# Kernel optimization log

Hardware: AMD Instinct MI355X
Metric: run time of the kernel (lower is better)

Reference implementation:

```python
import jax, jax.numpy as jnp
import numpy as np

SEMA_DIM = 1024
L1, L2, B = 256, 320, 64


def setup_inputs() -> dict:
    key = jax.random.key(0)
    k1, k2, kw1, kb1, kw2, kb2 = jax.random.split(key, 6)
    D = SEMA_DIM
    s = 1.0 / np.sqrt(D)
    return {
        "r1": jax.random.normal(k1, (L1, B, D), dtype=jnp.float32),
        "r2": jax.random.normal(k2, (L2, B, D), dtype=jnp.float32),
        "W1": jax.random.uniform(kw1, (D, D), jnp.float32, -s, s),
        "b1": jax.random.uniform(kb1, (D,), jnp.float32, -s, s),
        "W2": jax.random.uniform(kw2, (D, D), jnp.float32, -s, s),
        "b2": jax.random.uniform(kb2, (D,), jnp.float32, -s, s),
    }


def _mlp(x, W1, b1, W2, b2):
    # torch Linear: x @ W.T + b
    h = jax.nn.relu(x @ W1.T + b1)
    return h @ W2.T + b2


def reference(r1, r2, W1, b1, W2, b2):
    # (L, B, D) -> mlp -> (B, L, D)
    r1 = jnp.transpose(_mlp(r1, W1, b1, W2, b2), (1, 0, 2))  # [B, L1, D]
    r2 = jnp.transpose(_mlp(r2, W1, b1, W2, b2), (1, 0, 2))  # [B, L2, D]

    o = jnp.einsum("bid,bjd->bij", r1, r2)  # [B, L1, L2]
    o1 = jax.nn.softmax(o, axis=2)           # attend r1 -> r2
    o2 = jax.nn.softmax(o, axis=1)           # attend r2 -> r1

    r1_c = jnp.einsum("bij,bjd->bid", o1, r2)  # [B, L1, D]
    r2_c = jnp.einsum("bij,bid->bjd", o2, r1)  # [B, L2, D]

    r1_pool = jnp.concatenate([r1, r1_c], axis=-1).sum(axis=1) / r1.shape[1]  # [B, 2D]
    r2_pool = jnp.concatenate([r2, r2_c], axis=-1).sum(axis=1) / r2.shape[1]  # [B, 2D]
    return (r1_pool, r2_pool)
```

## Files before the change

kernel.cpp:

```cpp
#include <hip/hip_runtime.h>
#include <stdint.h>

#define L1C 256
#define L2C 320
#define BC  64
#define DC  1024

typedef __bf16 bf16_t;
typedef __bf16 bf16x8 __attribute__((ext_vector_type(8)));
typedef __bf16 bf16x4 __attribute__((ext_vector_type(4)));
typedef float  f32x4  __attribute__((ext_vector_type(4)));

__device__ __forceinline__ void gload16(const void* g, void* l) {
  __builtin_amdgcn_global_load_lds(
      (__attribute__((address_space(1))) void*)g,
      (__attribute__((address_space(3))) void*)l, 16, 0, 0);
}

__global__ __launch_bounds__(256)
void prep_kernel(const float* __restrict__ r1, const float* __restrict__ r2,
                 bf16_t* __restrict__ XB,
                 const float* __restrict__ W1, bf16_t* __restrict__ WB1,
                 const float* __restrict__ W2, bf16_t* __restrict__ WB2,
                 bf16_t* __restrict__ W2T,
                 const float* __restrict__ b2, float* __restrict__ w2b,
                 float* __restrict__ zb) {
  __shared__ float buf[32 * 33];
  const int b = (int)blockIdx.x;
  if (b < 9216) {
    const float* src;
    size_t soff;
    if (b < 4096) { src = r1; soff = (size_t)b * 1024; }
    else          { src = r2; soff = (size_t)(b - 4096) * 1024; }
    const size_t doff = (size_t)b * 1024;
#pragma unroll
    for (int k = 0; k < 4; ++k) {
      const int i = threadIdx.x + k * 256;
      float4 v = ((const float4*)src)[soff + i];
      bf16x4 o = { (__bf16)v.x, (__bf16)v.y, (__bf16)v.z, (__bf16)v.w };
      ((bf16x4*)XB)[doff + i] = o;
    }
  } else if (b < 9728) {
    const int bb = b - 9216;
    const float* src = (bb < 256) ? W1 : W2;
    bf16_t* dst = (bb < 256) ? WB1 : WB2;
    const size_t base = (size_t)(bb & 255) * 1024;
#pragma unroll
    for (int k = 0; k < 4; ++k) {
      const int i = threadIdx.x + k * 256;
      float4 v = ((const float4*)src)[base + i];
      bf16x4 o = { (__bf16)v.x, (__bf16)v.y, (__bf16)v.z, (__bf16)v.w };
      ((bf16x4*)dst)[base + i] = o;
    }
  } else if (b < 10752) {
    const int bb = b - 9728;
    float (*tile)[33] = (float(*)[33])buf;
    const int tx = threadIdx.x & 31, ty = threadIdx.x >> 5;
    const int x0 = (bb & 31) * 32, y0 = (bb >> 5) * 32;
#pragma unroll
    for (int k = 0; k < 32; k += 8)
      tile[ty + k][tx] = W2[(size_t)(y0 + ty + k) * 1024 + x0 + tx];
    __syncthreads();
#pragma unroll
    for (int k = 0; k < 32; k += 8)
      W2T[(size_t)(x0 + ty + k) * 1024 + y0 + tx] = (bf16_t)tile[tx][ty + k];
  } else if (b < 10816) {
    const int bb = b - 10752;
    float (*red)[17] = (float(*)[17])buf;
    const int dt = threadIdx.x & 15, kg = threadIdx.x >> 4;
    const int d = bb * 16 + dt;
    float s = 0.f;
    for (int k = kg * 64; k < kg * 64 + 64; ++k)
      s += W2[(size_t)k * 1024 + d] * b2[k];
    red[kg][dt] = s;
    __syncthreads();
    if (kg == 0) {
      float t = 0.f;
#pragma unroll
      for (int g = 0; g < 16; ++g) t += red[g][dt];
      w2b[d] = t;
    }
  } else {
#pragma unroll
    for (int k = 0; k < 4; ++k) zb[threadIdx.x + k * 256] = 0.f;
  }
}

__global__ __launch_bounds__(256, 3)
void gemm1_128(const bf16_t* __restrict__ A, const bf16_t* __restrict__ W,
               const float* __restrict__ bias, bf16_t* __restrict__ C) {
  const int wg = ((int)blockIdx.x & 7) * 288 + ((int)blockIdx.x >> 3);
  const int mt = wg >> 3, nt = wg & 7;

  __shared__ __align__(16) char lds[49152];

  const int t = threadIdx.x;
  const int lane = t & 63, w = t >> 6;
  const int sRow = t >> 2;
  const int sCol8 = (((t & 3) ^ ((t >> 3) & 3))) * 8;
  const int t16 = t * 16;

  const bf16_t* A0 = A + (size_t)(mt * 128 + sRow) * 1024 + sCol8;
  const bf16_t* A1 = A0 + (size_t)64 * 1024;
  const bf16_t* B0 = W + (size_t)(nt * 128 + sRow) * 1024 + sCol8;
  const bf16_t* B1 = B0 + (size_t)64 * 1024;

  const int wr = (w >> 1) * 64, wc = (w & 1) * 64;
  const int rsel = lane & 15, hi = lane >> 4;
  const int kchunk = (hi ^ ((rsel >> 1) & 3)) << 4;
  const int offA = ((wr + rsel) << 6) + kchunk;
  const int offB = 8192 + ((wc + rsel) << 6) + kchunk;

  f32x4 acc[4][4] = {};

#pragma unroll
  for (int p = 0; p < 2; ++p) {
    char* db = lds + p * 16384;
    gload16(A0 + p * 32, db + t16);
    gload16(A1 + p * 32, db + 4096 + t16);
    gload16(B0 + p * 32, db + 8192 + t16);
    gload16(B1 + p * 32, db + 12288 + t16);
  }
  asm volatile("s_waitcnt vmcnt(4)" ::: "memory");
  __builtin_amdgcn_s_barrier();
  __builtin_amdgcn_sched_barrier(0);

  int cur = 0;
#pragma unroll 1
  for (int tt = 0; tt < 32; ++tt) {
    const char* rb = lds + cur * 16384;
    int nx = cur + 2; if (nx >= 3) nx -= 3;
    char* sb = lds + nx * 16384;
    const int ks = (tt + 2) * 32;
    bf16x8 af[4], bfv[4];
#pragma unroll
    for (int m = 0; m < 4; ++m) af[m] = *(const bf16x8*)(rb + offA + m * 1024);
#pragma unroll
    for (int n = 0; n < 4; ++n) bfv[n] = *(const bf16x8*)(rb + offB + n * 1024);
    if (tt < 30) {
      gload16(A0 + ks, sb + t16);
      gload16(A1 + ks, sb + 4096 + t16);
      gload16(B0 + ks, sb + 8192 + t16);
      gload16(B1 + ks, sb + 12288 + t16);
    }
    __builtin_amdgcn_s_setprio(1);
#pragma unroll
    for (int m = 0; m < 4; ++m)
#pragma unroll
      for (int n = 0; n < 4; ++n)
        acc[m][n] = __builtin_amdgcn_mfma_f32_16x16x32_bf16(af[m], bfv[n], acc[m][n], 0, 0, 0);
    __builtin_amdgcn_s_setprio(0);
    if (tt < 30)       asm volatile("s_waitcnt vmcnt(4)" ::: "memory");
    else if (tt == 30) asm volatile("s_waitcnt vmcnt(0)" ::: "memory");
    __builtin_amdgcn_s_barrier();
    __builtin_amdgcn_sched_barrier(0);
    cur = (cur + 1 == 3) ? 0 : cur + 1;
  }

  const int row0 = mt * 128 + wr + hi * 4;
  const int col0 = nt * 128 + wc + rsel;
  float bv[4];
#pragma unroll
  for (int n = 0; n < 4; ++n) bv[n] = bias[col0 + n * 16];
#pragma unroll
  for (int m = 0; m < 4; ++m) {
#pragma unroll
    for (int q = 0; q < 4; ++q) {
      const size_t rr = (size_t)(row0 + m * 16 + q) * 1024;
#pragma unroll
      for (int n = 0; n < 4; ++n) {
        float v = fmaxf(acc[m][n][q] + bv[n], 0.f);
        C[rr + col0 + n * 16] = (bf16_t)v;
      }
    }
  }
}

__global__ __launch_bounds__(256)
void tg_kernel(const bf16_t* __restrict__ H, const float* __restrict__ w2b,
               float* __restrict__ tT1, float* __restrict__ tT2,
               const bf16_t* __restrict__ W2T, float* __restrict__ Gpart) {
  __shared__ __align__(16) bf16_t sA[128 * 32];
  __shared__ __align__(16) bf16_t sB[128 * 32];
  const int blk = (int)blockIdx.x;
  if (blk >= 256) {
    const int wv = threadIdx.x >> 6, lane = threadIdx.x & 63;
    const int r = (blk - 256) * 4 + wv;
    const bf16_t* hrow = H + (size_t)r * 1024;
    float s = 0.f;
#pragma unroll
    for (int h = 0; h < 2; ++h) {
      bf16x8 v = *(const bf16x8*)(hrow + h * 512 + lane * 8);
#pragma unroll
      for (int e = 0; e < 8; ++e) s += (float)v[e] * w2b[h * 512 + lane * 8 + e];
    }
#pragma unroll
    for (int off = 32; off; off >>= 1) s += __shfl_xor(s, off);
    if (lane == 0) {
      const int b = r & 63;
      if (r < 16384) tT1[b * L1C + (r >> 6)] = s;
      else           tT2[b * L2C + ((r - 16384) >> 6)] = s;
    }
    return;
  }
  const int slice = blk >> 6;
  const int tl = blk & 63;
  const int mt = tl >> 3, nt = tl & 7;
  const int koff = slice * 256;

  const int f = threadIdx.x;
  const int lane = f & 63, w = f >> 6;
  const int sRow = f >> 2, sCol8 = (f & 3) * 8;

  const bf16_t* Ab = W2T + (size_t)mt * 128 * 1024 + (size_t)sRow * 1024 + sCol8;
  const bf16_t* Bb = W2T + (size_t)nt * 128 * 1024 + (size_t)sRow * 1024 + sCol8;

  bf16_t* sAp = sA + sRow * 32 + sCol8;
  bf16_t* sBp = sB + sRow * 32 + sCol8;

  const int wr = (w >> 1) * 64, wc = (w & 1) * 64;
  const int rsel = lane & 15, koff2 = (lane >> 4) * 8;
  const bf16_t* rA = sA + (wr + rsel) * 32 + koff2;
  const bf16_t* rB = sB + (wc + rsel) * 32 + koff2;

  f32x4 acc[4][4] = {};
  for (int kt = koff; kt < koff + 256; kt += 32) {
    __syncthreads();
    gload16(Ab + kt,             sAp);
    gload16(Ab + kt + 64 * 1024, sAp + 64 * 32);
    gload16(Bb + kt,             sBp);
    gload16(Bb + kt + 64 * 1024, sBp + 64 * 32);
    asm volatile("s_waitcnt vmcnt(0)" ::: "memory");
    __syncthreads();
    bf16x8 af[4], bfv[4];
#pragma unroll
    for (int m = 0; m < 4; ++m) af[m] = *(const bf16x8*)(rA + m * 16 * 32);
#pragma unroll
    for (int n = 0; n < 4; ++n) bfv[n] = *(const bf16x8*)(rB + n * 16 * 32);
#pragma unroll
    for (int m = 0; m < 4; ++m)
#pragma unroll
      for (int n = 0; n < 4; ++n)
        acc[m][n] = __builtin_amdgcn_mfma_f32_16x16x32_bf16(af[m], bfv[n], acc[m][n], 0, 0, 0);
  }

  float* Pb = Gpart + (size_t)slice * 1048576;
  const int row0 = mt * 128 + wr + (lane >> 4) * 4;
  const int col0 = nt * 128 + wc + rsel;
#pragma unroll
  for (int n = 0; n < 4; ++n) {
    const int c = col0 + n * 16;
#pragma unroll
    for (int m = 0; m < 4; ++m) {
      const int r = row0 + m * 16;
#pragma unroll
      for (int q = 0; q < 4; ++q)
        Pb[(size_t)(r + q) * 1024 + c] = acc[m][n][q];
    }
  }
}

__global__ __launch_bounds__(256)
void g_reduce(const float* __restrict__ Gp, bf16_t* __restrict__ GB) {
  const int i4 = blockIdx.x * 256 + threadIdx.x;
  float4 a = ((const float4*)Gp)[i4];
  float4 b = ((const float4*)(Gp + 1048576))[i4];
  float4 c = ((const float4*)(Gp + 2097152))[i4];
  float4 d = ((const float4*)(Gp + 3145728))[i4];
  bf16x4 o = { (bf16_t)(a.x + b.x + c.x + d.x), (bf16_t)(a.y + b.y + c.y + d.y),
               (bf16_t)(a.z + b.z + c.z + d.z), (bf16_t)(a.w + b.w + c.w + d.w) };
  ((bf16x4*)GB)[i4] = o;
}

__global__ __launch_bounds__(512, 2)
void mlp_gemm8(const bf16_t* __restrict__ A, const bf16_t* __restrict__ W,
               const float* __restrict__ bias, bf16_t* __restrict__ C,
               int Mtiles, int relu) {
  const int nwg = Mtiles * 4;
  const int cpx = nwg >> 3;
  const int wg  = ((int)blockIdx.x & 7) * cpx + ((int)blockIdx.x >> 3);
  const int mt = wg >> 2, nt = wg & 3;

  __shared__ __align__(16) char lds[131072];

  const int t    = threadIdx.x;
  const int lane = t & 63, wid = t >> 6;
  const int wm = wid >> 2, wn = wid & 3;
  const int rsel = lane & 15, hi = lane >> 4;
  const int t16 = t * 16;

  const int P0 = t16, P1 = 8192 + t16;
  const int Lg0 = P0 ^ ((P0 >> 3) & 0x30);
  const int Lg1 = P1 ^ ((P1 >> 3) & 0x30);
  const int rS0 = Lg0 >> 6, cS0 = (Lg0 & 63) >> 1;
  const int rS1 = Lg1 >> 6, cS1 = (Lg1 & 63) >> 1;
  const bf16_t* pA0 = A + (size_t)(mt * 256 + rS0) * 1024 + cS0;
  const bf16_t* pA1 = A + (size_t)(mt * 256 + rS1) * 1024 + cS1;
  const bf16_t* pB0 = W + (size_t)(nt * 256 + rS0) * 1024 + cS0;
  const bf16_t* pB1 = W + (size_t)(nt * 256 + rS1) * 1024 + cS1;

  const int kchunk = (hi ^ ((rsel >> 1) & 3)) << 4;
  const int offA = ((wm * 128 + rsel) << 6) + kchunk;
  const int offB = 16384 + ((wn * 64 + rsel) << 6) + kchunk;

  f32x4 acc[8][4] = {};
  bf16x8 bfr[4];

#pragma unroll
  for (int p = 0; p < 3; ++p) {
    char* db = lds + p * 32768;
    gload16(pA0 + p * 32, db + t16);
    gload16(pA1 + p * 32, db + 8192 + t16);
    gload16(pB0 + p * 32, db + 16384 + t16);
    gload16(pB1 + p * 32, db + 24576 + t16);
  }
  asm volatile("s_waitcnt vmcnt(8)" ::: "memory");
  __builtin_amdgcn_s_barrier();
  __builtin_amdgcn_sched_barrier(0);

#pragma unroll 1
  for (int tt = 0; tt < 32; ++tt) {
    const char* rb = lds + (tt & 3) * 32768;
    char* sb = lds + ((tt + 3) & 3) * 32768;
    const int ks = (tt + 3) * 32;
    bf16x8 af[4];
#pragma unroll
    for (int m = 0; m < 4; ++m) af[m] = *(const bf16x8*)(rb + offA + m * 1024);
#pragma unroll
    for (int n = 0; n < 4; ++n) bfr[n] = *(const bf16x8*)(rb + offB + n * 1024);
    if (tt < 29) {
      gload16(pA0 + ks, sb + t16);
      gload16(pA1 + ks, sb + 8192 + t16);
    }
    __builtin_amdgcn_s_setprio(1);
#pragma unroll
    for (int m = 0; m < 4; ++m)
#pragma unroll
      for (int n = 0; n < 4; ++n)
        acc[m][n] = __builtin_amdgcn_mfma_f32_16x16x32_bf16(af[m], bfr[n], acc[m][n], 0, 0, 0);
    __builtin_amdgcn_s_setprio(0);
    __builtin_amdgcn_s_barrier();
    __builtin_amdgcn_sched_barrier(0);
#pragma unroll
    for (int m = 0; m < 4; ++m) af[m] = *(const bf16x8*)(rb + offA + (m + 4) * 1024);
    if (tt < 29) {
      gload16(pB0 + ks, sb + 16384 + t16);
      gload16(pB1 + ks, sb + 24576 + t16);
    }
    __builtin_amdgcn_s_setprio(1);
#pragma unroll
    for (int m = 0; m < 4; ++m)
#pragma unroll
      for (int n = 0; n < 4; ++n)
        acc[m + 4][n] = __builtin_amdgcn_mfma_f32_16x16x32_bf16(af[m], bfr[n], acc[m + 4][n], 0, 0, 0);
    __builtin_amdgcn_s_setprio(0);
    if (tt < 29)       asm volatile("s_waitcnt vmcnt(8)" ::: "memory");
    else if (tt == 29) asm volatile("s_waitcnt vmcnt(4)" ::: "memory");
    else if (tt == 30) asm volatile("s_waitcnt vmcnt(0)" ::: "memory");
    __builtin_amdgcn_s_barrier();
    __builtin_amdgcn_sched_barrier(0);
  }

  const int row0 = mt * 256 + wm * 128 + hi * 4;
  const int col0 = nt * 256 + wn * 64 + rsel;
  float bv[4];
#pragma unroll
  for (int n = 0; n < 4; ++n) bv[n] = bias[col0 + n * 16];
#pragma unroll
  for (int m = 0; m < 8; ++m) {
#pragma unroll
    for (int q = 0; q < 4; ++q) {
      const size_t rr = (size_t)(row0 + m * 16 + q) * 1024;
#pragma unroll
      for (int n = 0; n < 4; ++n) {
        float v = acc[m][n][q] + bv[n];
        if (relu) v = fmaxf(v, 0.f);
        C[rr + col0 + n * 16] = (bf16_t)v;
      }
    }
  }
}

__global__ __launch_bounds__(256)
void pool_gemmK(const bf16_t* __restrict__ A, const bf16_t* __restrict__ W,
                float* __restrict__ P) {
  const int slice = (int)blockIdx.x >> 4;
  const int tl = (int)blockIdx.x & 15;
  const int mt = tl >> 3, nt = tl & 7;
  const int koff = slice * 128;

  const int f = threadIdx.x;
  const int lane = f & 63, w = f >> 6;
  const int sRow = f >> 2, sCol8 = (f & 3) * 8;

  const bf16_t* Ab = A + (size_t)mt * 128 * 1024 + (size_t)sRow * 1024 + sCol8;
  const bf16_t* Bb = W + (size_t)nt * 128 * 1024 + (size_t)sRow * 1024 + sCol8;

  __shared__ __align__(16) bf16_t sA[128 * 32];
  __shared__ __align__(16) bf16_t sB[128 * 32];
  bf16_t* sAp = sA + sRow * 32 + sCol8;
  bf16_t* sBp = sB + sRow * 32 + sCol8;

  const int wr = (w >> 1) * 64, wc = (w & 1) * 64;
  const int rsel = lane & 15, koff2 = (lane >> 4) * 8;
  const bf16_t* rA = sA + (wr + rsel) * 32 + koff2;
  const bf16_t* rB = sB + (wc + rsel) * 32 + koff2;

  f32x4 acc[4][4] = {};
  for (int kt = koff; kt < koff + 128; kt += 32) {
    __syncthreads();
    gload16(Ab + kt,             sAp);
    gload16(Ab + kt + 64 * 1024, sAp + 64 * 32);
    gload16(Bb + kt,             sBp);
    gload16(Bb + kt + 64 * 1024, sBp + 64 * 32);
    asm volatile("s_waitcnt vmcnt(0)" ::: "memory");
    __syncthreads();
    bf16x8 af[4], bfv[4];
#pragma unroll
    for (int m = 0; m < 4; ++m) af[m] = *(const bf16x8*)(rA + m * 16 * 32);
#pragma unroll
    for (int n = 0; n < 4; ++n) bfv[n] = *(const bf16x8*)(rB + n * 16 * 32);
#pragma unroll
    for (int m = 0; m < 4; ++m)
#pragma unroll
      for (int n = 0; n < 4; ++n)
        acc[m][n] = __builtin_amdgcn_mfma_f32_16x16x32_bf16(af[m], bfv[n], acc[m][n], 0, 0, 0);
  }

  float* Pb = P + (size_t)slice * 262144;
  const int row0 = mt * 128 + wr + (lane >> 4) * 4;
  const int col0 = nt * 128 + wc + rsel;
#pragma unroll
  for (int n = 0; n < 4; ++n) {
    const int c = col0 + n * 16;
#pragma unroll
    for (int m = 0; m < 4; ++m) {
      const int r = row0 + m * 16;
#pragma unroll
      for (int q = 0; q < 4; ++q)
        Pb[(size_t)(r + q) * 1024 + c] = acc[m][n][q];
    }
  }
}

__global__ __launch_bounds__(256)
void pool_reduce(const float* __restrict__ Pp, const float* __restrict__ b2,
                 float* __restrict__ out) {
  const int idx = blockIdx.x * 256 + threadIdx.x;
  const int r = idx >> 10, c = idx & 1023;
  float s = b2[c];
#pragma unroll
  for (int sl = 0; sl < 8; ++sl) s += Pp[(size_t)sl * 262144 + idx];
  const int g = r >> 6, b = r & 63;
  out[(size_t)(g >> 1) * 131072 + (size_t)b * 2048 + (g & 1) * 1024 + c] = s;
}

__global__ __launch_bounds__(256)
void logits_gemm(const bf16_t* __restrict__ Y1, const bf16_t* __restrict__ Y2,
                 float* __restrict__ O) {
  const int wg = ((int)blockIdx.x & 7) * 48 + ((int)blockIdx.x >> 3);
  const int b = wg / 6, t6 = wg % 6;
  const int mt = t6 / 3, nt = t6 % 3;

  __shared__ __align__(16) char lds[65536];

  const int t = threadIdx.x;
  const int lane = t & 63, w = t >> 6;
  const int sRow = t >> 2;
  const int sCol8 = (((t & 3) ^ ((t >> 3) & 3))) * 8;
  const int t16 = t * 16;

  const int i0 = mt * 128 + sRow;
  const int i1 = i0 + 64;
  int j0 = nt * 128 + sRow;      if (j0 > L2C - 1) j0 = L2C - 1;
  int j1 = nt * 128 + sRow + 64; if (j1 > L2C - 1) j1 = L2C - 1;
  const bf16_t* A0 = Y1 + ((size_t)i0 * BC + b) * DC + sCol8;
  const bf16_t* A1 = Y1 + ((size_t)i1 * BC + b) * DC + sCol8;
  const bf16_t* B0 = Y2 + ((size_t)j0 * BC + b) * DC + sCol8;
  const bf16_t* B1 = Y2 + ((size_t)j1 * BC + b) * DC + sCol8;

  const int wr = (w >> 1) * 64, wc = (w & 1) * 64;
  const int rsel = lane & 15, hi = lane >> 4;
  const int kchunk = (hi ^ ((rsel >> 1) & 3)) << 4;
  const int offA = ((wr + rsel) << 6) + kchunk;
  const int offB = 8192 + ((wc + rsel) << 6) + kchunk;

  f32x4 acc[4][4] = {};

#pragma unroll
  for (int p = 0; p < 3; ++p) {
    char* db = lds + p * 16384;
    gload16(A0 + p * 32, db + t16);
    gload16(A1 + p * 32, db + 4096 + t16);
    gload16(B0 + p * 32, db + 8192 + t16);
    gload16(B1 + p * 32, db + 12288 + t16);
  }
  asm volatile("s_waitcnt vmcnt(8)" ::: "memory");
  __builtin_amdgcn_s_barrier();
  __builtin_amdgcn_sched_barrier(0);

#pragma unroll 1
  for (int tt = 0; tt < 32; ++tt) {
    const char* rb = lds + (tt & 3) * 16384;
    char* sb = lds + ((tt + 3) & 3) * 16384;
    const int ks = (tt + 3) * 32;
    bf16x8 af[4], bfv[4];
#pragma unroll
    for (int m = 0; m < 4; ++m) af[m] = *(const bf16x8*)(rb + offA + m * 1024);
#pragma unroll
    for (int n = 0; n < 4; ++n) bfv[n] = *(const bf16x8*)(rb + offB + n * 1024);
    if (tt < 29) {
      gload16(A0 + ks, sb + t16);
      gload16(A1 + ks, sb + 4096 + t16);
      gload16(B0 + ks, sb + 8192 + t16);
      gload16(B1 + ks, sb + 12288 + t16);
    }
    __builtin_amdgcn_s_setprio(1);
#pragma unroll
    for (int m = 0; m < 4; ++m)
#pragma unroll
      for (int n = 0; n < 4; ++n)
        acc[m][n] = __builtin_amdgcn_mfma_f32_16x16x32_bf16(af[m], bfv[n], acc[m][n], 0, 0, 0);
    __builtin_amdgcn_s_setprio(0);
    if (tt < 29)       asm volatile("s_waitcnt vmcnt(8)" ::: "memory");
    else if (tt == 29) asm volatile("s_waitcnt vmcnt(4)" ::: "memory");
    else if (tt == 30) asm volatile("s_waitcnt vmcnt(0)" ::: "memory");
    __builtin_amdgcn_s_barrier();
    __builtin_amdgcn_sched_barrier(0);
  }

  float* Ob = O + (size_t)b * L1C * L2C;
  const int row0 = mt * 128 + wr + hi * 4;
  const int col0 = nt * 128 + wc + rsel;
#pragma unroll
  for (int n = 0; n < 4; ++n) {
    const int c = col0 + n * 16;
    if (c < L2C) {
#pragma unroll
      for (int m = 0; m < 4; ++m) {
        const int r = row0 + m * 16;
#pragma unroll
        for (int q = 0; q < 4; ++q)
          Ob[(size_t)(r + q) * L2C + c] = acc[m][n][q];
      }
    }
  }
}

__global__ __launch_bounds__(256)
void row_stats(const float* __restrict__ O, const float* __restrict__ tT2,
               float* __restrict__ rowM, float* __restrict__ rowInv) {
  const int gw = blockIdx.x * 4 + (threadIdx.x >> 6);
  const int lane = threadIdx.x & 63;
  const int b = gw >> 8;
  const float* row = O + (size_t)gw * L2C;
  const float* t2 = tT2 + b * L2C;
  float v[5];
  float m = -1e30f;
#pragma unroll
  for (int t = 0; t < 5; ++t) { v[t] = row[t * 64 + lane] + t2[t * 64 + lane]; m = fmaxf(m, v[t]); }
#pragma unroll
  for (int off = 32; off; off >>= 1) m = fmaxf(m, __shfl_xor(m, off));
  float s = 0.f;
#pragma unroll
  for (int t = 0; t < 5; ++t) s += __expf(v[t] - m);
#pragma unroll
  for (int off = 32; off; off >>= 1) s += __shfl_xor(s, off);
  if (lane == 0) { rowM[gw] = m; rowInv[gw] = 1.f / s; }
}

__global__ __launch_bounds__(256)
void col_stats_c1(const float* __restrict__ O, const float* __restrict__ tT1,
                  const float* __restrict__ tT2,
                  const float* __restrict__ rowM, const float* __restrict__ rowInv,
                  float* __restrict__ colM, float* __restrict__ colInv,
                  float* __restrict__ c1) {
  const int b = blockIdx.x / 5, jb = blockIdx.x % 5;
  const int jl = threadIdx.x & 63, ig = threadIdx.x >> 6;
  const int j = jb * 64 + jl;
  const float* Ob = O + (size_t)b * L1C * L2C + j;
  const float* rM = rowM + b * L1C;
  const float* rI = rowInv + b * L1C;
  const float* t1 = tT1 + b * L1C;
  const float t2j = tT2[b * L2C + j];
  float m = -1e30f, s = 0.f, cp = 0.f;
  for (int i = ig; i < L1C; i += 4) {
    float ov = Ob[(size_t)i * L2C];
    float v = ov + t1[i];
    float mn = fmaxf(m, v);
    s = s * __expf(m - mn) + __expf(v - mn);
    m = mn;
    cp += __expf(ov + t2j - rM[i]) * rI[i];
  }
  __shared__ float sm[4][64], ss[4][64], sc[4][64];
  sm[ig][jl] = m; ss[ig][jl] = s; sc[ig][jl] = cp;
  __syncthreads();
  if (ig == 0) {
    for (int g = 1; g < 4; ++g) {
      float mg = sm[g][jl], sg = ss[g][jl];
      float mn = fmaxf(m, mg);
      s = s * __expf(m - mn) + sg * __expf(mg - mn);
      m = mn;
      cp += sc[g][jl];
    }
    colM[b * L2C + j] = m;
    colInv[b * L2C + j] = 1.f / s;
    c1[b * L2C + j] = cp;
  }
}

__global__ __launch_bounds__(256)
void c2_kernel(const float* __restrict__ O, const float* __restrict__ tT1,
               const float* __restrict__ colM, const float* __restrict__ colInv,
               float* __restrict__ c2) {
  const int gw = blockIdx.x * 4 + (threadIdx.x >> 6);
  const int lane = threadIdx.x & 63;
  const int b = gw >> 8;
  const float* row = O + (size_t)gw * L2C;
  const float* cM = colM + b * L2C;
  const float* cI = colInv + b * L2C;
  const float t1i = tT1[b * L1C + (gw & 255)];
  float s = 0.f;
#pragma unroll
  for (int t = 0; t < 5; ++t) {
    const int j = t * 64 + lane;
    s += __expf(row[j] + t1i - cM[j]) * cI[j];
  }
#pragma unroll
  for (int off = 32; off; off >>= 1) s += __shfl_xor(s, off);
  if (lane == 0) c2[gw] = s;
}

__global__ __launch_bounds__(256)
void u_kernel(const bf16_t* __restrict__ H, const float* __restrict__ c1,
              const float* __restrict__ c2, bf16_t* __restrict__ Ub) {
  const int b = blockIdx.x >> 2;
  const int d = (blockIdx.x & 3) * 256 + threadIdx.x;
  const bf16_t* H2 = H + (size_t)L1C * BC * DC;
  float s1 = 0.f, s1c = 0.f, s2 = 0.f, s2c = 0.f;
  const float* c2b = c2 + b * L1C;
  for (int i = 0; i < L1C; ++i) {
    float v = (float)H[((size_t)i * BC + b) * DC + d];
    s1 += v; s1c += c2b[i] * v;
  }
  const float* c1b = c1 + b * L2C;
  for (int j = 0; j < L2C; ++j) {
    float v = (float)H2[((size_t)j * BC + b) * DC + d];
    s2 += v; s2c += c1b[j] * v;
  }
  Ub[(size_t)(0 * 64 + b) * 1024 + d] = (bf16_t)(s1  * (1.f / L1C));
  Ub[(size_t)(1 * 64 + b) * 1024 + d] = (bf16_t)(s2c * (1.f / L1C));
  Ub[(size_t)(2 * 64 + b) * 1024 + d] = (bf16_t)(s2  * (1.f / L2C));
  Ub[(size_t)(3 * 64 + b) * 1024 + d] = (bf16_t)(s1c * (1.f / L2C));
}

extern "C" void kernel_launch(void* const* d_in, const int* in_sizes, int n_in,
                              void* d_out, int out_size, void* d_ws, size_t ws_size,
                              hipStream_t stream) {
  const float* r1 = (const float*)d_in[0];
  const float* r2 = (const float*)d_in[1];
  const float* W1 = (const float*)d_in[2];
  const float* b1 = (const float*)d_in[3];
  const float* W2 = (const float*)d_in[4];
  const float* b2 = (const float*)d_in[5];
  float* out = (float*)d_out;
  char* ws = (char*)d_ws;

  const size_t M1 = (size_t)L1C * BC;
  const size_t M2 = (size_t)L2C * BC;
  const size_t Mt = M1 + M2;

  size_t off = 0;
  bf16_t* XB  = (bf16_t*)(ws + off); off += Mt * DC * 2;
  bf16_t* HB  = (bf16_t*)(ws + off); off += Mt * DC * 2;
  bf16_t* WB1 = (bf16_t*)(ws + off); off += (size_t)DC * DC * 2;
  bf16_t* WB2 = (bf16_t*)(ws + off); off += (size_t)DC * DC * 2;
  bf16_t* W2T = (bf16_t*)(ws + off); off += (size_t)DC * DC * 2;
  bf16_t* GB  = (bf16_t*)(ws + off); off += (size_t)DC * DC * 2;
  float* w2b   = (float*)(ws + off); off += 4096;
  float* zb    = (float*)(ws + off); off += 4096;
  float* tT1   = (float*)(ws + off); off += BC * L1C * 4;
  float* tT2   = (float*)(ws + off); off += BC * L2C * 4;
  float* rowM  = (float*)(ws + off); off += BC * L1C * 4;
  float* rowIv = (float*)(ws + off); off += BC * L1C * 4;
  float* colM  = (float*)(ws + off); off += BC * L2C * 4;
  float* colIv = (float*)(ws + off); off += BC * L2C * 4;
  float* c1v   = (float*)(ws + off); off += BC * L2C * 4;
  float* c2v   = (float*)(ws + off); off += BC * L1C * 4;
  bf16_t* Ub   = (bf16_t*)(ws + off); off += 256 * DC * 2;

  bf16_t* Z = XB;
  float*  O = (float*)((char*)XB + 35651584);
  float*  Gpart = (float*)((char*)XB + 58720256);
  float*  Ppart = (float*)HB;
  bf16_t* H2 = HB + M1 * DC;

  prep_kernel<<<10817, 256, 0, stream>>>(r1, r2, XB, W1, WB1, W2, WB2, W2T,
                                         b2, w2b, zb);

  gemm1_128<<<2304, 256, 0, stream>>>(XB, WB1, b1, HB);

  tg_kernel<<<9472, 256, 0, stream>>>(HB, w2b, tT1, tT2, W2T, Gpart);
  g_reduce<<<1024, 256, 0, stream>>>(Gpart, GB);

  mlp_gemm8<<<256, 512, 0, stream>>>(HB, GB, zb, Z, 64, 0);

  logits_gemm<<<384, 256, 0, stream>>>(Z, H2, O);

  row_stats<<<4096, 256, 0, stream>>>(O, tT2, rowM, rowIv);
  col_stats_c1<<<320, 256, 0, stream>>>(O, tT1, tT2, rowM, rowIv, colM, colIv, c1v);
  c2_kernel<<<4096, 256, 0, stream>>>(O, tT1, colM, colIv, c2v);

  u_kernel<<<256, 256, 0, stream>>>(HB, c1v, c2v, Ub);
  pool_gemmK<<<128, 256, 0, stream>>>(Ub, WB2, Ppart);
  pool_reduce<<<1024, 256, 0, stream>>>(Ppart, b2, out);
}
```

Before: 282.6 us.

## Fold W2ᵀW2 Gram GEMM into first-layer GEMM launch and drop split-K reduce

The Gram matrix GEMM (W2T·W2T) no longer runs as a 4-way split-K inside tg_kernel. It now runs as 64 extra full-K blocks prepended to the first MLP GEMM launch, and those blocks write bf16 GB directly. This removes the fp32 partial buffer, the g_reduce kernel and one launch, and lets the Gram GEMM overlap with the large H GEMM. The cost is 64 long-running blocks with 32 K-iterations each, which could form a tail, plus a separate t_kernel launch for the row-dot products.

```diff
diff --git a/kernel.cpp b/kernel.cpp
--- a/kernel.cpp
+++ b/kernel.cpp
@@ -87,12 +87,65 @@
 }
 
 __global__ __launch_bounds__(256, 3)
-void gemm1_128(const bf16_t* __restrict__ A, const bf16_t* __restrict__ W,
-               const float* __restrict__ bias, bf16_t* __restrict__ C) {
-  const int wg = ((int)blockIdx.x & 7) * 288 + ((int)blockIdx.x >> 3);
+void g1g_kernel(const bf16_t* __restrict__ A, const bf16_t* __restrict__ W,
+                const float* __restrict__ bias, bf16_t* __restrict__ C,
+                const bf16_t* __restrict__ W2T, bf16_t* __restrict__ GB) {
+  __shared__ __align__(16) char lds[49152];
+  const int blk = (int)blockIdx.x;
+
+  if (blk < 64) {
+    bf16_t* sA = (bf16_t*)lds;
+    bf16_t* sB = (bf16_t*)(lds + 8192);
+    const int f = threadIdx.x;
+    const int lane = f & 63, w4 = f >> 6;
+    const int sRowG = f >> 2, sCol8G = (f & 3) * 8;
+    const bf16_t* Ab = W2T + (size_t)(blk >> 3) * 128 * 1024 + (size_t)sRowG * 1024 + sCol8G;
+    const bf16_t* Bb = W2T + (size_t)(blk & 7) * 128 * 1024 + (size_t)sRowG * 1024 + sCol8G;
+    bf16_t* sAp = sA + sRowG * 32 + sCol8G;
+    bf16_t* sBp = sB + sRowG * 32 + sCol8G;
+    const int wrG = (w4 >> 1) * 64, wcG = (w4 & 1) * 64;
+    const int rselG = lane & 15, koff2 = (lane >> 4) * 8;
+    const bf16_t* rA = sA + (wrG + rselG) * 32 + koff2;
+    const bf16_t* rB = sB + (wcG + rselG) * 32 + koff2;
+    f32x4 acc[4][4] = {};
+    for (int kt = 0; kt < 1024; kt += 32) {
+      __syncthreads();
+      gload16(Ab + kt,             sAp);
+      gload16(Ab + kt + 64 * 1024, sAp + 64 * 32);
+      gload16(Bb + kt,             sBp);
+      gload16(Bb + kt + 64 * 1024, sBp + 64 * 32);
+      asm volatile("s_waitcnt vmcnt(0)" ::: "memory");
+      __syncthreads();
+      bf16x8 af[4], bfv[4];
+#pragma unroll
+      for (int m = 0; m < 4; ++m) af[m] = *(const bf16x8*)(rA + m * 16 * 32);
+#pragma unroll
+      for (int n = 0; n < 4; ++n) bfv[n] = *(const bf16x8*)(rB + n * 16 * 32);
+#pragma unroll
+      for (int m = 0; m < 4; ++m)
+#pragma unroll
+        for (int n = 0; n < 4; ++n)
+          acc[m][n] = __builtin_amdgcn_mfma_f32_16x16x32_bf16(af[m], bfv[n], acc[m][n], 0, 0, 0);
+    }
+    const int row0 = (blk >> 3) * 128 + wrG + (lane >> 4) * 4;
+    const int col0 = (blk & 7) * 128 + wcG + rselG;
+#pragma unroll
+    for (int n = 0; n < 4; ++n) {
+      const int c = col0 + n * 16;
+#pragma unroll
+      for (int m = 0; m < 4; ++m) {
+        const int r = row0 + m * 16;
+#pragma unroll
+        for (int q = 0; q < 4; ++q)
+          GB[(size_t)(r + q) * 1024 + c] = (bf16_t)acc[m][n][q];
+      }
+    }
+    return;
+  }
+
+  const int bid = blk - 64;
+  const int wg = (bid & 7) * 288 + (bid >> 3);
   const int mt = wg >> 3, nt = wg & 7;
-
-  __shared__ __align__(16) char lds[49152];
 
   const int t = threadIdx.x;
   const int lane = t & 63, w = t >> 6;
@@ -177,99 +230,25 @@
 }
 
 __global__ __launch_bounds__(256)
-void tg_kernel(const bf16_t* __restrict__ H, const float* __restrict__ w2b,
-               float* __restrict__ tT1, float* __restrict__ tT2,
-               const bf16_t* __restrict__ W2T, float* __restrict__ Gpart) {
-  __shared__ __align__(16) bf16_t sA[128 * 32];
-  __shared__ __align__(16) bf16_t sB[128 * 32];
-  const int blk = (int)blockIdx.x;
-  if (blk >= 256) {
-    const int wv = threadIdx.x >> 6, lane = threadIdx.x & 63;
-    const int r = (blk - 256) * 4 + wv;
-    const bf16_t* hrow = H + (size_t)r * 1024;
-    float s = 0.f;
-#pragma unroll
-    for (int h = 0; h < 2; ++h) {
-      bf16x8 v = *(const bf16x8*)(hrow + h * 512 + lane * 8);
-#pragma unroll
-      for (int e = 0; e < 8; ++e) s += (float)v[e] * w2b[h * 512 + lane * 8 + e];
-    }
-#pragma unroll
-    for (int off = 32; off; off >>= 1) s += __shfl_xor(s, off);
-    if (lane == 0) {
-      const int b = r & 63;
-      if (r < 16384) tT1[b * L1C + (r >> 6)] = s;
-      else           tT2[b * L2C + ((r - 16384) >> 6)] = s;
-    }
-    return;
-  }
-  const int slice = blk >> 6;
-  const int tl = blk & 63;
-  const int mt = tl >> 3, nt = tl & 7;
-  const int koff = slice * 256;
-
-  const int f = threadIdx.x;
-  const int lane = f & 63, w = f >> 6;
-  const int sRow = f >> 2, sCol8 = (f & 3) * 8;
-
-  const bf16_t* Ab = W2T + (size_t)mt * 128 * 1024 + (size_t)sRow * 1024 + sCol8;
-  const bf16_t* Bb = W2T + (size_t)nt * 128 * 1024 + (size_t)sRow * 1024 + sCol8;
-
-  bf16_t* sAp = sA + sRow * 32 + sCol8;
-  bf16_t* sBp = sB + sRow * 32 + sCol8;
-
-  const int wr = (w >> 1) * 64, wc = (w & 1) * 64;
-  const int rsel = lane & 15, koff2 = (lane >> 4) * 8;
-  const bf16_t* rA = sA + (wr + rsel) * 32 + koff2;
-  const bf16_t* rB = sB + (wc + rsel) * 32 + koff2;
-
-  f32x4 acc[4][4] = {};
-  for (int kt = koff; kt < koff + 256; kt += 32) {
-    __syncthreads();
-    gload16(Ab + kt,             sAp);
-    gload16(Ab + kt + 64 * 1024, sAp + 64 * 32);
-    gload16(Bb + kt,             sBp);
-    gload16(Bb + kt + 64 * 1024, sBp + 64 * 32);
-    asm volatile("s_waitcnt vmcnt(0)" ::: "memory");
-    __syncthreads();
-    bf16x8 af[4], bfv[4];
-#pragma unroll
-    for (int m = 0; m < 4; ++m) af[m] = *(const bf16x8*)(rA + m * 16 * 32);
-#pragma unroll
-    for (int n = 0; n < 4; ++n) bfv[n] = *(const bf16x8*)(rB + n * 16 * 32);
-#pragma unroll
-    for (int m = 0; m < 4; ++m)
-#pragma unroll
-      for (int n = 0; n < 4; ++n)
-        acc[m][n] = __builtin_amdgcn_mfma_f32_16x16x32_bf16(af[m], bfv[n], acc[m][n], 0, 0, 0);
-  }
-
-  float* Pb = Gpart + (size_t)slice * 1048576;
-  const int row0 = mt * 128 + wr + (lane >> 4) * 4;
-  const int col0 = nt * 128 + wc + rsel;
-#pragma unroll
-  for (int n = 0; n < 4; ++n) {
-    const int c = col0 + n * 16;
-#pragma unroll
-    for (int m = 0; m < 4; ++m) {
-      const int r = row0 + m * 16;
-#pragma unroll
-      for (int q = 0; q < 4; ++q)
-        Pb[(size_t)(r + q) * 1024 + c] = acc[m][n][q];
-    }
-  }
-}
-
-__global__ __launch_bounds__(256)
-void g_reduce(const float* __restrict__ Gp, bf16_t* __restrict__ GB) {
-  const int i4 = blockIdx.x * 256 + threadIdx.x;
-  float4 a = ((const float4*)Gp)[i4];
-  float4 b = ((const float4*)(Gp + 1048576))[i4];
-  float4 c = ((const float4*)(Gp + 2097152))[i4];
-  float4 d = ((const float4*)(Gp + 3145728))[i4];
-  bf16x4 o = { (bf16_t)(a.x + b.x + c.x + d.x), (bf16_t)(a.y + b.y + c.y + d.y),
-               (bf16_t)(a.z + b.z + c.z + d.z), (bf16_t)(a.w + b.w + c.w + d.w) };
-  ((bf16x4*)GB)[i4] = o;
+void t_kernel(const bf16_t* __restrict__ H, const float* __restrict__ w2b,
+              float* __restrict__ tT1, float* __restrict__ tT2) {
+  const int wv = threadIdx.x >> 6, lane = threadIdx.x & 63;
+  const int r = blockIdx.x * 4 + wv;
+  const bf16_t* hrow = H + (size_t)r * 1024;
+  float s = 0.f;
+#pragma unroll
+  for (int h = 0; h < 2; ++h) {
+    bf16x8 v = *(const bf16x8*)(hrow + h * 512 + lane * 8);
+#pragma unroll
+    for (int e = 0; e < 8; ++e) s += (float)v[e] * w2b[h * 512 + lane * 8 + e];
+  }
+#pragma unroll
+  for (int off = 32; off; off >>= 1) s += __shfl_xor(s, off);
+  if (lane == 0) {
+    const int b = r & 63;
+    if (r < 16384) tT1[b * L1C + (r >> 6)] = s;
+    else           tT2[b * L2C + ((r - 16384) >> 6)] = s;
+  }
 }
 
 __global__ __launch_bounds__(512, 2)
@@ -691,17 +670,15 @@
 
   bf16_t* Z = XB;
   float*  O = (float*)((char*)XB + 35651584);
-  float*  Gpart = (float*)((char*)XB + 58720256);
   float*  Ppart = (float*)HB;
   bf16_t* H2 = HB + M1 * DC;
 
   prep_kernel<<<10817, 256, 0, stream>>>(r1, r2, XB, W1, WB1, W2, WB2, W2T,
                                          b2, w2b, zb);
 
-  gemm1_128<<<2304, 256, 0, stream>>>(XB, WB1, b1, HB);
-
-  tg_kernel<<<9472, 256, 0, stream>>>(HB, w2b, tT1, tT2, W2T, Gpart);
-  g_reduce<<<1024, 256, 0, stream>>>(Gpart, GB);
+  g1g_kernel<<<2368, 256, 0, stream>>>(XB, WB1, b1, HB, W2T, GB);
+
+  t_kernel<<<9216, 256, 0, stream>>>(HB, w2b, tT1, tT2);
 
   mlp_gemm8<<<256, 512, 0, stream>>>(HB, GB, zb, Z, 64, 0);
 
```

Result: no change. 277.1 us (median of 2 runs) (-2.0%).
